# Kernel tuning notes

Hardware: AMD Instinct MI355X
Metric: run time of the kernel (lower is better)

## Reference

```python
import jax, jax.numpy as jnp
import numpy as np

NUM_CLASSES = 10000
EMBED_LEN_DECODER = 100
DECODER_EMBEDDING = 768
DUPLICATE_FACTOR = int(NUM_CLASSES / EMBED_LEN_DECODER + 0.999)  # 100
BATCH = 512


def setup_inputs() -> dict:
    key = jax.random.key(0)
    k_h, k_w = jax.random.split(key)
    h = jax.random.normal(k_h, (BATCH, EMBED_LEN_DECODER, DECODER_EMBEDDING), dtype=jnp.float32)
    # xavier_normal over (decoder_embedding, duplicate_factor) fan dims
    std = (2.0 / (DECODER_EMBEDDING + DUPLICATE_FACTOR)) ** 0.5
    duplicate_pooling = std * jax.random.normal(
        k_w, (EMBED_LEN_DECODER, DECODER_EMBEDDING, DUPLICATE_FACTOR), dtype=jnp.float32)
    bias = jnp.zeros((NUM_CLASSES,), dtype=jnp.float32)
    return {"h": h, "duplicate_pooling": duplicate_pooling, "bias": bias}


def reference(h, duplicate_pooling, bias):
    # per-group batched matmul: out[b, i, f] = sum_d h[b, i, d] * W[i, d, f]
    out_extrap = jnp.einsum('bid,idf->bif', h, duplicate_pooling)
    # flatten groups, truncate to num_classes, add bias
    logits = out_extrap.reshape(h.shape[0], -1)[:, :NUM_CLASSES] + bias
    return logits
```

## Files before the change

kernel.cpp:

```cpp
#include <hip/hip_runtime.h>

typedef __attribute__((ext_vector_type(4))) float f32x4;
typedef __attribute__((ext_vector_type(8))) __bf16 bf16x8;
typedef __attribute__((ext_vector_type(8))) unsigned short ushort8v;
typedef __attribute__((ext_vector_type(4))) unsigned short ushort4v;

#define NGRP   100
#define DDIM   768
#define FDIM   100
#define NCLS   10000
#define NSTEP  12
#define NTILE  7
#define NCHUNK 14
#define CH_SHORTS 512
#define STEP_SHORTS (NCHUNK * CH_SHORTS)
#define G_SHORTS (NSTEP * STEP_SHORTS)

#define GLOBAL_AS __attribute__((address_space(1)))
#define LDS_AS    __attribute__((address_space(3)))

static __device__ __forceinline__ unsigned short f2bf(float f) {
    __bf16 b = (__bf16)f;
    return __builtin_bit_cast(unsigned short, b);
}

__global__ __launch_bounds__(256) void build_wt(
    const float* __restrict__ W, unsigned short* __restrict__ Wt)
{
    __shared__ unsigned short lt[FDIM * 66];
    const int b = blockIdx.x, g = b / 12, step = b % 12;
    const int tid = threadIdx.x;

    const float* Wg = W + (size_t)g * (DDIM * FDIM) + (size_t)step * 64 * FDIM;
#pragma unroll
    for (int j = 0; j < 25; ++j) {
        const int i = tid + j * 256;
        const int r = i / 100, f = i % 100;
        lt[f * 66 + r] = f2bf(Wg[i]);
    }
    __syncthreads();

    unsigned short* out = Wt + (size_t)g * G_SHORTS + step * STEP_SHORTS;
#pragma unroll
    for (int j = 0; j < 4; ++j) {
        const int idx = tid + j * 256;
        if (idx < NCHUNK * 64) {
            const int c = idx >> 6, lane = idx & 63;
            const int t = c >> 1, half = c & 1;
            int f = t * 16 + (lane & 15); if (f > FDIM - 1) f = FDIM - 1;
            const int kk = half * 32 + (lane >> 4) * 8;
            const unsigned short* src = &lt[f * 66 + kk];
            ushort8v v;
            v[0]=src[0]; v[1]=src[1]; v[2]=src[2]; v[3]=src[3];
            v[4]=src[4]; v[5]=src[5]; v[6]=src[6]; v[7]=src[7];
            *(ushort8v*)(out + (size_t)idx * 8) = v;
        }
    }
}

__global__ __launch_bounds__(256, 4) void gfcp_main(
    const float* __restrict__ H, const unsigned short* __restrict__ Wt,
    const float* __restrict__ Bv, float* __restrict__ Out)
{
    __shared__ unsigned short Bl[2][STEP_SHORTS];

    const int bid  = blockIdx.x;
    const int wgid = (bid & 7) * 100 + (bid >> 3);
    const int g    = wgid >> 3;
    const int m0   = (wgid & 7) * 64;

    const int tid  = threadIdx.x;
    const int lane = tid & 63;
    const int wv   = tid >> 6;
    const int r16  = lane & 15;
    const int kg   = lane >> 4;

    const float* Ap = H + (size_t)(m0 + wv * 16 + r16) * (NGRP * DDIM)
                        + (size_t)g * DDIM + kg * 8;
    const unsigned short* Bg = Wt + (size_t)g * G_SHORTS + lane * 8;

    f32x4 acc[NTILE];
#pragma unroll
    for (int t = 0; t < NTILE; ++t) acc[t] = (f32x4)(0.0f);

    f32x4 a[2][4];

    auto stage = [&](int buf, int step) {
        const unsigned short* gsrc = Bg + step * STEP_SHORTS;
#pragma unroll
        for (int i = 0; i < 4; ++i) {
            const int c = wv + i * 4;
            if (c < NCHUNK) {
                __builtin_amdgcn_global_load_lds(
                    (const GLOBAL_AS void*)(gsrc + c * CH_SHORTS),
                    (LDS_AS void*)(&Bl[buf][c * CH_SHORTS]),
                    16, 0, 0);
            }
        }
    };
    auto loadA = [&](int slot, int step) {
        const float* p = Ap + step * 64;
        a[slot][0] = *(const f32x4*)(p);
        a[slot][1] = *(const f32x4*)(p + 4);
        a[slot][2] = *(const f32x4*)(p + 32);
        a[slot][3] = *(const f32x4*)(p + 36);
    };
    auto compute = [&](int buf, int slot) {
        const unsigned short* bl = &Bl[buf][0];
#pragma unroll
        for (int s = 0; s < 2; ++s) {
            const f32x4 x = a[slot][2 * s], y = a[slot][2 * s + 1];
            ushort8v u;
            u[0]=f2bf(x[0]); u[1]=f2bf(x[1]); u[2]=f2bf(x[2]); u[3]=f2bf(x[3]);
            u[4]=f2bf(y[0]); u[5]=f2bf(y[1]); u[6]=f2bf(y[2]); u[7]=f2bf(y[3]);
            const bf16x8 af = __builtin_bit_cast(bf16x8, u);
#pragma unroll
            for (int t = 0; t < NTILE; ++t) {
                const ushort8v bu = *(const ushort8v*)(bl + (t * 2 + s) * CH_SHORTS + lane * 8);
                acc[t] = __builtin_amdgcn_mfma_f32_16x16x32_bf16(
                    af, __builtin_bit_cast(bf16x8, bu), acc[t], 0, 0, 0);
            }
        }
    };

    loadA(0, 0);
    loadA(1, 1);
    stage(0, 0);
    __syncthreads();

#pragma unroll
    for (int t = 0; t < NSTEP; ++t) {
        const int cur = t & 1;
        if (t + 1 < NSTEP) stage(cur ^ 1, t + 1);
        compute(cur, cur);
        if (t + 2 < NSTEP) loadA(cur, t + 2);
        if (t + 1 < NSTEP) __syncthreads();
    }

    const int orow  = m0 + wv * 16 + kg * 4;
    const int fbase = g * FDIM;
#pragma unroll
    for (int t = 0; t < NTILE; ++t) {
        const int fc = t * 16 + r16;
        if (fc < FDIM) {
            const float bv = Bv[fbase + fc];
#pragma unroll
            for (int r = 0; r < 4; ++r) {
                Out[(size_t)(orow + r) * NCLS + fbase + fc] = acc[t][r] + bv;
            }
        }
    }
}

extern "C" void kernel_launch(void* const* d_in, const int* in_sizes, int n_in,
                              void* d_out, int out_size, void* d_ws, size_t ws_size,
                              hipStream_t stream) {
    const float* H  = (const float*)d_in[0];
    const float* W  = (const float*)d_in[1];
    const float* Bv = (const float*)d_in[2];
    float* Out = (float*)d_out;
    unsigned short* Wt = (unsigned short*)d_ws;

    build_wt<<<dim3(1200), dim3(256), 0, stream>>>(W, Wt);
    gfcp_main<<<dim3(800), dim3(256), 0, stream>>>(H, Wt, Bv, Out);
}
```

Before: 50.19 us.

## Halve waves per block, give each wave two M-tiles, use fine-grained waitcnt barriers

The main kernel now runs two waves per block instead of four, and each wave computes two 16-row M tiles. This reuses every B fragment read from LDS for two MFMAs and halves LDS read traffic per MFMA. __syncthreads is replaced with explicit s_waitcnt vmcnt(8) plus s_barrier and sched_barriers, so the prefetched A loads can stay in flight across the barrier. The cost is more registers per thread and fewer waves per block, which may reduce latency hiding.

```diff
diff --git a/kernel.cpp b/kernel.cpp
--- a/kernel.cpp
+++ b/kernel.cpp
@@ -3,7 +3,6 @@
 typedef __attribute__((ext_vector_type(4))) float f32x4;
 typedef __attribute__((ext_vector_type(8))) __bf16 bf16x8;
 typedef __attribute__((ext_vector_type(8))) unsigned short ushort8v;
-typedef __attribute__((ext_vector_type(4))) unsigned short ushort4v;
 
 #define NGRP   100
 #define DDIM   768
@@ -58,7 +57,7 @@
     }
 }
 
-__global__ __launch_bounds__(256, 4) void gfcp_main(
+__global__ __launch_bounds__(128, 3) void gfcp_main(
     const float* __restrict__ H, const unsigned short* __restrict__ Wt,
     const float* __restrict__ Bv, float* __restrict__ Out)
 {
@@ -75,78 +74,105 @@
     const int r16  = lane & 15;
     const int kg   = lane >> 4;
 
-    const float* Ap = H + (size_t)(m0 + wv * 16 + r16) * (NGRP * DDIM)
-                        + (size_t)g * DDIM + kg * 8;
+    const float* Ap0 = H + (size_t)(m0 + wv * 32 + r16) * (NGRP * DDIM)
+                         + (size_t)g * DDIM + kg * 8;
+    const float* Ap1 = Ap0 + (size_t)16 * (NGRP * DDIM);
     const unsigned short* Bg = Wt + (size_t)g * G_SHORTS + lane * 8;
 
-    f32x4 acc[NTILE];
+    f32x4 acc[2][NTILE];
 #pragma unroll
-    for (int t = 0; t < NTILE; ++t) acc[t] = (f32x4)(0.0f);
+    for (int at = 0; at < 2; ++at)
+#pragma unroll
+        for (int t = 0; t < NTILE; ++t) acc[at][t] = (f32x4)(0.0f);
 
-    f32x4 a[2][4];
+    f32x4 a[2][2][4];
 
     auto stage = [&](int buf, int step) {
         const unsigned short* gsrc = Bg + step * STEP_SHORTS;
 #pragma unroll
-        for (int i = 0; i < 4; ++i) {
-            const int c = wv + i * 4;
-            if (c < NCHUNK) {
-                __builtin_amdgcn_global_load_lds(
-                    (const GLOBAL_AS void*)(gsrc + c * CH_SHORTS),
-                    (LDS_AS void*)(&Bl[buf][c * CH_SHORTS]),
-                    16, 0, 0);
-            }
+        for (int i = 0; i < 7; ++i) {
+            const int c = wv * 7 + i;
+            __builtin_amdgcn_global_load_lds(
+                (const GLOBAL_AS void*)(gsrc + c * CH_SHORTS),
+                (LDS_AS void*)(&Bl[buf][c * CH_SHORTS]),
+                16, 0, 0);
         }
     };
     auto loadA = [&](int slot, int step) {
-        const float* p = Ap + step * 64;
-        a[slot][0] = *(const f32x4*)(p);
-        a[slot][1] = *(const f32x4*)(p + 4);
-        a[slot][2] = *(const f32x4*)(p + 32);
-        a[slot][3] = *(const f32x4*)(p + 36);
+        const float* p0 = Ap0 + step * 64;
+        a[slot][0][0] = *(const f32x4*)(p0);
+        a[slot][0][1] = *(const f32x4*)(p0 + 4);
+        a[slot][0][2] = *(const f32x4*)(p0 + 32);
+        a[slot][0][3] = *(const f32x4*)(p0 + 36);
+        const float* p1 = Ap1 + step * 64;
+        a[slot][1][0] = *(const f32x4*)(p1);
+        a[slot][1][1] = *(const f32x4*)(p1 + 4);
+        a[slot][1][2] = *(const f32x4*)(p1 + 32);
+        a[slot][1][3] = *(const f32x4*)(p1 + 36);
     };
     auto compute = [&](int buf, int slot) {
         const unsigned short* bl = &Bl[buf][0];
 #pragma unroll
         for (int s = 0; s < 2; ++s) {
-            const f32x4 x = a[slot][2 * s], y = a[slot][2 * s + 1];
-            ushort8v u;
-            u[0]=f2bf(x[0]); u[1]=f2bf(x[1]); u[2]=f2bf(x[2]); u[3]=f2bf(x[3]);
-            u[4]=f2bf(y[0]); u[5]=f2bf(y[1]); u[6]=f2bf(y[2]); u[7]=f2bf(y[3]);
-            const bf16x8 af = __builtin_bit_cast(bf16x8, u);
+            ushort8v u0, u1;
+#pragma unroll
+            for (int j = 0; j < 4; ++j) {
+                u0[j]   = f2bf(a[slot][0][2*s][j]); u0[j+4] = f2bf(a[slot][0][2*s+1][j]);
+                u1[j]   = f2bf(a[slot][1][2*s][j]); u1[j+4] = f2bf(a[slot][1][2*s+1][j]);
+            }
+            const bf16x8 af0 = __builtin_bit_cast(bf16x8, u0);
+            const bf16x8 af1 = __builtin_bit_cast(bf16x8, u1);
 #pragma unroll
             for (int t = 0; t < NTILE; ++t) {
                 const ushort8v bu = *(const ushort8v*)(bl + (t * 2 + s) * CH_SHORTS + lane * 8);
-                acc[t] = __builtin_amdgcn_mfma_f32_16x16x32_bf16(
-                    af, __builtin_bit_cast(bf16x8, bu), acc[t], 0, 0, 0);
+                const bf16x8 bf = __builtin_bit_cast(bf16x8, bu);
+                acc[0][t] = __builtin_amdgcn_mfma_f32_16x16x32_bf16(af0, bf, acc[0][t], 0, 0, 0);
+                acc[1][t] = __builtin_amdgcn_mfma_f32_16x16x32_bf16(af1, bf, acc[1][t], 0, 0, 0);
             }
         }
     };
 
     loadA(0, 0);
+    __builtin_amdgcn_sched_barrier(0);
+    stage(0, 0);
+    __builtin_amdgcn_sched_barrier(0);
     loadA(1, 1);
-    stage(0, 0);
-    __syncthreads();
+    __builtin_amdgcn_sched_barrier(0);
+    asm volatile("s_waitcnt vmcnt(8)" ::: "memory");
+    __builtin_amdgcn_s_barrier();
+    __builtin_amdgcn_sched_barrier(0);
 
 #pragma unroll
     for (int t = 0; t < NSTEP; ++t) {
         const int cur = t & 1;
-        if (t + 1 < NSTEP) stage(cur ^ 1, t + 1);
+        if (t + 1 < NSTEP) {
+            stage(cur ^ 1, t + 1);
+            __builtin_amdgcn_sched_barrier(0);
+        }
         compute(cur, cur);
         if (t + 2 < NSTEP) loadA(cur, t + 2);
-        if (t + 1 < NSTEP) __syncthreads();
+        if (t + 1 < NSTEP) {
+            __builtin_amdgcn_sched_barrier(0);
+            if (t + 2 < NSTEP) asm volatile("s_waitcnt vmcnt(8)" ::: "memory");
+            else               asm volatile("s_waitcnt vmcnt(0)" ::: "memory");
+            __builtin_amdgcn_s_barrier();
+            __builtin_amdgcn_sched_barrier(0);
+        }
     }
 
-    const int orow  = m0 + wv * 16 + kg * 4;
     const int fbase = g * FDIM;
 #pragma unroll
-    for (int t = 0; t < NTILE; ++t) {
-        const int fc = t * 16 + r16;
-        if (fc < FDIM) {
-            const float bv = Bv[fbase + fc];
+    for (int at = 0; at < 2; ++at) {
+        const int orow = m0 + wv * 32 + at * 16 + kg * 4;
 #pragma unroll
-            for (int r = 0; r < 4; ++r) {
-                Out[(size_t)(orow + r) * NCLS + fbase + fc] = acc[t][r] + bv;
+        for (int t = 0; t < NTILE; ++t) {
+            const int fc = t * 16 + r16;
+            if (fc < FDIM) {
+                const float bv = Bv[fbase + fc];
+#pragma unroll
+                for (int r = 0; r < 4; ++r) {
+                    Out[(size_t)(orow + r) * NCLS + fbase + fc] = acc[at][t][r] + bv;
+                }
             }
         }
     }
@@ -162,5 +188,5 @@
     unsigned short* Wt = (unsigned short*)d_ws;
 
     build_wt<<<dim3(1200), dim3(256), 0, stream>>>(W, Wt);
-    gfcp_main<<<dim3(800), dim3(256), 0, stream>>>(H, Wt, Bv, Out);
+    gfcp_main<<<dim3(800), dim3(128), 0, stream>>>(H, Wt, Bv, Out);
 }
```

Measured after the change: 50.29 us. Within noise of the previous version (+0.2%).

## Replace LDS-staged weight tiles with per-wave register double-buffering

Applied to the files above, without the earlier changes.

Switches the main GEMM from 4-wave workgroups that share weight tiles through LDS (global_load_lds plus barriers) to single-wave workgroups that load weight fragments directly into registers with double buffering. The grid grows fourfold and all __syncthreads are removed. This aims to cut barrier stalls and LDS round-trips. In exchange, each wave fetches its own copy of the weights, quadrupling weight traffic through L2, and register pressure rises sharply.

```diff
diff --git a/kernel.cpp b/kernel.cpp
--- a/kernel.cpp
+++ b/kernel.cpp
@@ -3,7 +3,6 @@
 typedef __attribute__((ext_vector_type(4))) float f32x4;
 typedef __attribute__((ext_vector_type(8))) __bf16 bf16x8;
 typedef __attribute__((ext_vector_type(8))) unsigned short ushort8v;
-typedef __attribute__((ext_vector_type(4))) unsigned short ushort4v;
 
 #define NGRP   100
 #define DDIM   768
@@ -15,9 +14,6 @@
 #define CH_SHORTS 512
 #define STEP_SHORTS (NCHUNK * CH_SHORTS)
 #define G_SHORTS (NSTEP * STEP_SHORTS)
-
-#define GLOBAL_AS __attribute__((address_space(1)))
-#define LDS_AS    __attribute__((address_space(3)))
 
 static __device__ __forceinline__ unsigned short f2bf(float f) {
     __bf16 b = (__bf16)f;
@@ -58,24 +54,20 @@
     }
 }
 
-__global__ __launch_bounds__(256, 4) void gfcp_main(
+__global__ __launch_bounds__(64, 2) void gfcp_main(
     const float* __restrict__ H, const unsigned short* __restrict__ Wt,
     const float* __restrict__ Bv, float* __restrict__ Out)
 {
-    __shared__ unsigned short Bl[2][STEP_SHORTS];
+    const int bid  = blockIdx.x;
+    const int wgid = (bid & 7) * 400 + (bid >> 3);
+    const int g    = wgid >> 5;
+    const int m0   = (wgid & 31) * 16;
 
-    const int bid  = blockIdx.x;
-    const int wgid = (bid & 7) * 100 + (bid >> 3);
-    const int g    = wgid >> 3;
-    const int m0   = (wgid & 7) * 64;
-
-    const int tid  = threadIdx.x;
-    const int lane = tid & 63;
-    const int wv   = tid >> 6;
+    const int lane = threadIdx.x & 63;
     const int r16  = lane & 15;
     const int kg   = lane >> 4;
 
-    const float* Ap = H + (size_t)(m0 + wv * 16 + r16) * (NGRP * DDIM)
+    const float* Ap = H + (size_t)(m0 + r16) * (NGRP * DDIM)
                         + (size_t)g * DDIM + kg * 8;
     const unsigned short* Bg = Wt + (size_t)g * G_SHORTS + lane * 8;
 
@@ -83,61 +75,61 @@
 #pragma unroll
     for (int t = 0; t < NTILE; ++t) acc[t] = (f32x4)(0.0f);
 
-    f32x4 a[2][4];
+    f32x4 a0[4], a1[4];
+    ushort8v b0[NCHUNK], b1[NCHUNK];
 
-    auto stage = [&](int buf, int step) {
-        const unsigned short* gsrc = Bg + step * STEP_SHORTS;
-#pragma unroll
-        for (int i = 0; i < 4; ++i) {
-            const int c = wv + i * 4;
-            if (c < NCHUNK) {
-                __builtin_amdgcn_global_load_lds(
-                    (const GLOBAL_AS void*)(gsrc + c * CH_SHORTS),
-                    (LDS_AS void*)(&Bl[buf][c * CH_SHORTS]),
-                    16, 0, 0);
-            }
-        }
-    };
-    auto loadA = [&](int slot, int step) {
-        const float* p = Ap + step * 64;
-        a[slot][0] = *(const f32x4*)(p);
-        a[slot][1] = *(const f32x4*)(p + 4);
-        a[slot][2] = *(const f32x4*)(p + 32);
-        a[slot][3] = *(const f32x4*)(p + 36);
-    };
-    auto compute = [&](int buf, int slot) {
-        const unsigned short* bl = &Bl[buf][0];
-#pragma unroll
-        for (int s = 0; s < 2; ++s) {
-            const f32x4 x = a[slot][2 * s], y = a[slot][2 * s + 1];
-            ushort8v u;
-            u[0]=f2bf(x[0]); u[1]=f2bf(x[1]); u[2]=f2bf(x[2]); u[3]=f2bf(x[3]);
-            u[4]=f2bf(y[0]); u[5]=f2bf(y[1]); u[6]=f2bf(y[2]); u[7]=f2bf(y[3]);
-            const bf16x8 af = __builtin_bit_cast(bf16x8, u);
-#pragma unroll
-            for (int t = 0; t < NTILE; ++t) {
-                const ushort8v bu = *(const ushort8v*)(bl + (t * 2 + s) * CH_SHORTS + lane * 8);
-                acc[t] = __builtin_amdgcn_mfma_f32_16x16x32_bf16(
-                    af, __builtin_bit_cast(bf16x8, bu), acc[t], 0, 0, 0);
-            }
-        }
-    };
+#define LOADA(SL, STEP) do { \
+        const float* p_ = Ap + (STEP) * 64; \
+        SL[0] = *(const f32x4*)(p_); \
+        SL[1] = *(const f32x4*)(p_ + 4); \
+        SL[2] = *(const f32x4*)(p_ + 32); \
+        SL[3] = *(const f32x4*)(p_ + 36); \
+    } while (0)
 
-    loadA(0, 0);
-    loadA(1, 1);
-    stage(0, 0);
-    __syncthreads();
+#define LOADB(SL, STEP) do { \
+        const unsigned short* q_ = Bg + (STEP) * STEP_SHORTS; \
+        _Pragma("unroll") \
+        for (int c_ = 0; c_ < NCHUNK; ++c_) \
+            SL[c_] = *(const ushort8v*)(q_ + c_ * CH_SHORTS); \
+    } while (0)
+
+#define COMPUTE(ASL, BSL) do { \
+        _Pragma("unroll") \
+        for (int s_ = 0; s_ < 2; ++s_) { \
+            ushort8v u_; \
+            _Pragma("unroll") \
+            for (int j_ = 0; j_ < 4; ++j_) { \
+                u_[j_]     = f2bf(ASL[2*s_][j_]); \
+                u_[j_ + 4] = f2bf(ASL[2*s_+1][j_]); \
+            } \
+            const bf16x8 af_ = __builtin_bit_cast(bf16x8, u_); \
+            _Pragma("unroll") \
+            for (int t_ = 0; t_ < NTILE; ++t_) { \
+                acc[t_] = __builtin_amdgcn_mfma_f32_16x16x32_bf16( \
+                    af_, __builtin_bit_cast(bf16x8, BSL[t_ * 2 + s_]), acc[t_], 0, 0, 0); \
+            } \
+        } \
+    } while (0)
+
+    LOADA(a0, 0);
+    LOADA(a1, 1);
+    LOADB(b0, 0);
 
 #pragma unroll
     for (int t = 0; t < NSTEP; ++t) {
-        const int cur = t & 1;
-        if (t + 1 < NSTEP) stage(cur ^ 1, t + 1);
-        compute(cur, cur);
-        if (t + 2 < NSTEP) loadA(cur, t + 2);
-        if (t + 1 < NSTEP) __syncthreads();
+        if (t + 1 < NSTEP) {
+            if ((t & 1) == 0) LOADB(b1, t + 1); else LOADB(b0, t + 1);
+        }
+        if ((t & 1) == 0) {
+            COMPUTE(a0, b0);
+            if (t + 2 < NSTEP) LOADA(a0, t + 2);
+        } else {
+            COMPUTE(a1, b1);
+            if (t + 2 < NSTEP) LOADA(a1, t + 2);
+        }
     }
 
-    const int orow  = m0 + wv * 16 + kg * 4;
+    const int orow  = m0 + kg * 4;
     const int fbase = g * FDIM;
 #pragma unroll
     for (int t = 0; t < NTILE; ++t) {
@@ -162,5 +154,5 @@
     unsigned short* Wt = (unsigned short*)d_ws;
 
     build_wt<<<dim3(1200), dim3(256), 0, stream>>>(W, Wt);
-    gfcp_main<<<dim3(800), dim3(256), 0, stream>>>(H, Wt, Bv, Out);
+    gfcp_main<<<dim3(3200), dim3(64), 0, stream>>>(H, Wt, Bv, Out);
 }
```

New measurement: 54.46 us. +8.5%, slower.
